# Kernel tuning notes

Hardware: AMD Instinct MI355X
Metric: run time of the kernel (lower is better)

## Reference

```python
import jax, jax.numpy as jnp
import numpy as np

D_MODEL = 256

def setup_inputs() -> dict:
    key = jax.random.key(0)
    k_x, k_wqkv, k_bqkv, k_wp, k_bp = jax.random.split(key, 5)
    B, T, d = 4, 4096, D_MODEL
    bound_qkv = 1.0 / np.sqrt(d)
    return {
        "x": jax.random.normal(k_x, (B, T, d), dtype=jnp.float32),
        "W_qkv": jax.random.uniform(k_wqkv, (d, 3 * d), jnp.float32, -bound_qkv, bound_qkv),
        "b_qkv": jax.random.uniform(k_bqkv, (3 * d,), jnp.float32, -bound_qkv, bound_qkv),
        "W_proj": jax.random.uniform(k_wp, (d, d), jnp.float32, -bound_qkv, bound_qkv),
        "b_proj": jax.random.uniform(k_bp, (d,), jnp.float32, -bound_qkv, bound_qkv),
    }

def reference(x, W_qkv, b_qkv, W_proj, b_proj):
    B, T, d = x.shape
    qkv = x @ W_qkv + b_qkv                       # (B, T, 3d)
    q, k, v = jnp.split(qkv, 3, axis=-1)          # each (B, T, d)
    scale = 1.0 / np.sqrt(d).astype(np.float32)
    scores = jnp.einsum('btd,bsd->bts', q, k) * scale   # (B, T, T)
    causal = jnp.tril(jnp.ones((T, T), dtype=bool))     # allowed positions
    scores = jnp.where(causal, scores, -jnp.inf)
    weights = jax.nn.softmax(scores, axis=-1)           # (B, T, T)
    ctx = jnp.einsum('bts,bsd->btd', weights, v)        # (B, T, d)
    return ctx @ W_proj + b_proj
```

## Files before the change

### kernel.cpp

```cpp
#include <hip/hip_runtime.h>
#include <math.h>

#define TT 4096
#define BB 4
#define DM 256
#define NSEG_B 80

typedef __attribute__((ext_vector_type(8))) short short8;
typedef __attribute__((ext_vector_type(4))) short short4v;
typedef __attribute__((ext_vector_type(4))) float f32x4;

#define MFMA16(a, b, c) __builtin_amdgcn_mfma_f32_16x16x32_bf16(a, b, c, 0, 0, 0)

#define GL2LDS(gp, lp) __builtin_amdgcn_global_load_lds( \
    (const __attribute__((address_space(1))) unsigned int*)(gp), \
    (__attribute__((address_space(3))) unsigned int*)(lp), 16, 0, 0)

__device__ __forceinline__ short f2b(float f) {
    union { float f; unsigned u; } v; v.f = f;
    unsigned r = v.u + 0x7FFFu + ((v.u >> 16) & 1u);
    return (short)(r >> 16);
}

__global__ __launch_bounds__(256) void transpose_cast2(
    const float* __restrict__ W1, short* __restrict__ Wt1,
    const float* __restrict__ W2, short* __restrict__ Wt2)
{
    __shared__ float T[64 * 68];
    const int tid = threadIdx.x;
    const int by = blockIdx.y;
    const float* W; short* Wt; int N, n0;
    if (by < 12) { W = W1; Wt = Wt1; N = 768; n0 = by * 64; }
    else         { W = W2; Wt = Wt2; N = 256; n0 = (by - 12) * 64; }
    const int k0 = blockIdx.x * 64;
#pragma unroll
    for (int it = 0; it < 4; ++it) {
        int idx = tid + it * 256;
        int r = idx >> 4, c4 = idx & 15;
        *(float4*)&T[r * 68 + c4 * 4] =
            *(const float4*)&W[(size_t)(k0 + r) * N + n0 + c4 * 4];
    }
    __syncthreads();
#pragma unroll
    for (int it = 0; it < 4; ++it) {
        int idx = tid + it * 256;
        int n = idx >> 4, c4 = idx & 15;
        short4v t;
#pragma unroll
        for (int j = 0; j < 4; ++j) t[j] = f2b(T[(c4 * 4 + j) * 68 + n]);
        *(short4v*)&Wt[(size_t)(n0 + n) * 256 + k0 + c4 * 4] = t;
    }
}

__global__ __launch_bounds__(256) void qkv_gemm(
    const float* __restrict__ x, const short* __restrict__ Bt,
    const float* __restrict__ bias, short* __restrict__ qkvb,
    short* __restrict__ VtG)
{
    __shared__ short As[16384];
    __shared__ short Bs[16384];
    __shared__ short Ts[64 * 72];

    const int tid = threadIdx.x;
    const int w = tid >> 6, lane = tid & 63;
    const int l15 = lane & 15, quad = lane >> 4;
    const int m0 = blockIdx.x * 64;
    const int nsup = blockIdx.y * 384;

#pragma unroll
    for (int it = 0; it < 8; ++it) {
        int idx = tid + it * 256;
        int row = ((idx >> 9) << 4) + (idx & 15);
        int col = ((idx >> 6) & 7) * 32 + ((idx >> 4) & 3) * 8;
        const float* src = &x[(size_t)(m0 + row) * 256 + col];
        float4 u = *(const float4*)src, u2 = *(const float4*)(src + 4);
        short8 t;
        t[0] = f2b(u.x);  t[1] = f2b(u.y);  t[2] = f2b(u.z);  t[3] = f2b(u.w);
        t[4] = f2b(u2.x); t[5] = f2b(u2.y); t[6] = f2b(u2.z); t[7] = f2b(u2.w);
        *(short8*)&As[idx * 8] = t;
    }

    for (int t6 = 0; t6 < 6; ++t6) {
        const int n0 = nsup + t6 * 64;
#pragma unroll
        for (int it = 0; it < 8; ++it) {
            int idx = tid + it * 256;
            int n = ((idx >> 9) << 4) + (idx & 15);
            int col = ((idx >> 6) & 7) * 32 + ((idx >> 4) & 3) * 8;
            *(short8*)&Bs[idx * 8] = *(const short8*)&Bt[(size_t)(n0 + n) * 256 + col];
        }
        __syncthreads();

        f32x4 acc[4];
#pragma unroll
        for (int t = 0; t < 4; ++t) acc[t] = (f32x4){0.f, 0.f, 0.f, 0.f};
#pragma unroll
        for (int k0 = 0; k0 < 8; ++k0) {
            short8 a = *(const short8*)&As[((w * 8 + k0) * 64 + lane) * 8];
#pragma unroll
            for (int nt = 0; nt < 4; ++nt) {
                short8 bb = *(const short8*)&Bs[((nt * 8 + k0) * 64 + lane) * 8];
                acc[nt] = MFMA16(a, bb, acc[nt]);
            }
        }

        if (n0 < 512) {
#pragma unroll
            for (int nt = 0; nt < 4; ++nt) {
                int n = n0 + nt * 16 + l15;
                float bv = bias[n];
#pragma unroll
                for (int r = 0; r < 4; ++r)
                    qkvb[(size_t)(m0 + w * 16 + quad * 4 + r) * 768 + n]
                        = f2b(acc[nt][r] + bv);
            }
            __syncthreads();
        } else {
#pragma unroll
            for (int nt = 0; nt < 4; ++nt) {
                int n = n0 + nt * 16 + l15;
                float bv = bias[n];
#pragma unroll
                for (int r = 0; r < 4; ++r)
                    Ts[(nt * 16 + l15) * 72 + w * 16 + quad * 4 + r]
                        = f2b(acc[nt][r] + bv);
            }
            __syncthreads();
            const int d  = tid >> 2;
            const int c  = tid & 3;
            short8 v0 = *(const short8*)&Ts[d * 72 + c * 16];
            short8 v1 = *(const short8*)&Ts[d * 72 + c * 16 + 8];
            const int bg = m0 >> 12, key0 = (m0 & 4095) + c * 16;
            short* dst = &VtG[((size_t)bg * 256 + (n0 - 512) + d) * 4096 + key0];
            *(short8*)dst = v0;
            *(short8*)(dst + 8) = v1;
        }
    }
}

__global__ __launch_bounds__(256, 2) void flash_mfma(
    const short* __restrict__ qkv,
    const short* __restrict__ VtG,
    float* __restrict__ Opart,
    float* __restrict__ L)
{
    __shared__ short Ks[2][8192];
    __shared__ short Vs[2][8192];
    __shared__ short Ps[4096];

    const int tid = threadIdx.x;
    const int w = tid >> 6, lane = tid & 63;
    const int l15 = lane & 15, quad = lane >> 4;

    const int b = blockIdx.x & 3;
    const int e = (NSEG_B - 1) - (blockIdx.x >> 2);
    const int lid = b * NSEG_B + e;
    int gg = 0;
    while (gg < 3 && e >= 4 * (gg + 1) * (gg + 2)) ++gg;
    int off = e - 4 * gg * (gg + 1);
    int qt = 8 * gg + off / (gg + 1);
    int s  = off - (off / (gg + 1)) * (gg + 1);
    const int kb_lo = s * 32;
    const int kb_hi = min(kb_lo + 32, 4 * (qt + 1));
    const int nunits = kb_hi - kb_lo;

    const size_t base = (size_t)b * TT * 768;
    const int row0 = qt * 128;

    short8 aq[2][8];
#pragma unroll
    for (int rs = 0; rs < 2; ++rs) {
        const short* qrow = &qkv[base + (size_t)(row0 + rs * 64 + w * 16 + l15) * 768 + quad * 8];
#pragma unroll
        for (int k0 = 0; k0 < 8; ++k0)
            aq[rs][k0] = *(const short8*)&qrow[k0 * 32];
    }

#pragma unroll
    for (int it = 0; it < 4; ++it) {
        int idx = tid + it * 256;
        int row = ((idx >> 9) << 4) + (idx & 15);
        int col = ((idx >> 6) & 7) * 32 + ((idx >> 4) & 3) * 8;
        GL2LDS(&qkv[base + (size_t)(kb_lo * 32 + row) * 768 + 256 + col], &Ks[0][idx * 8]);
        int d  = ((idx >> 6) << 4) + (idx & 15);
        int kc = ((idx >> 4) & 3) * 8;
        GL2LDS(&VtG[((size_t)b * 256 + d) * 4096 + kb_lo * 32 + kc], &Vs[0][idx * 8]);
    }

    f32x4 o[2][16];
#pragma unroll
    for (int rs = 0; rs < 2; ++rs)
#pragma unroll
        for (int c = 0; c < 16; ++c) o[rs][c] = (f32x4){0.f, 0.f, 0.f, 0.f};
    float l_acc[2][4] = {{0.f, 0.f, 0.f, 0.f}, {0.f, 0.f, 0.f, 0.f}};

    for (int u = 0; u < nunits; ++u) {
        const int p = u & 1;
        const int j0 = (kb_lo + u) * 32;

        __syncthreads();

        if (u + 1 < nunits) {
            const int j0n = j0 + 32;
#pragma unroll
            for (int it = 0; it < 4; ++it) {
                int idx = tid + it * 256;
                int row = ((idx >> 9) << 4) + (idx & 15);
                int col = ((idx >> 6) & 7) * 32 + ((idx >> 4) & 3) * 8;
                GL2LDS(&qkv[base + (size_t)(j0n + row) * 768 + 256 + col], &Ks[p ^ 1][idx * 8]);
                int d  = ((idx >> 6) << 4) + (idx & 15);
                int kc = ((idx >> 4) & 3) * 8;
                GL2LDS(&VtG[((size_t)b * 256 + d) * 4096 + j0n + kc], &Vs[p ^ 1][idx * 8]);
            }
        }

        f32x4 s4[2][2];
#pragma unroll
        for (int rs = 0; rs < 2; ++rs)
#pragma unroll
            for (int nt = 0; nt < 2; ++nt) s4[rs][nt] = (f32x4){0.f, 0.f, 0.f, 0.f};
#pragma unroll
        for (int k0 = 0; k0 < 8; ++k0) {
#pragma unroll
            for (int nt = 0; nt < 2; ++nt) {
                short8 bb = *(const short8*)&Ks[p][((nt * 8 + k0) * 64 + lane) * 8];
                s4[0][nt] = MFMA16(aq[0][k0], bb, s4[0][nt]);
                s4[1][nt] = MFMA16(aq[1][k0], bb, s4[1][nt]);
            }
        }

#pragma unroll
        for (int rs = 0; rs < 2; ++rs) {
#pragma unroll
            for (int r = 0; r < 4; ++r) {
                const int rg = row0 + rs * 64 + w * 16 + quad * 4 + r;
#pragma unroll
                for (int nt = 0; nt < 2; ++nt) {
                    int jg = j0 + nt * 16 + l15;
                    float xx = s4[rs][nt][r] * 0.0625f;
                    if (jg > rg) xx = -INFINITY;
                    float pv = __expf(fminf(xx, 30.f));
                    l_acc[rs][r] += pv;
                    Ps[((rs * 4 + w) * 64 + (nt * 2 + (l15 >> 3)) * 16 + quad * 4 + r) * 8
                       + (l15 & 7)] = f2b(pv);
                }
            }
        }

        {
            short8 a0 = *(const short8*)&Ps[((0 * 4 + w) * 64 + lane) * 8];
            short8 a1 = *(const short8*)&Ps[((1 * 4 + w) * 64 + lane) * 8];
#pragma unroll
            for (int ct = 0; ct < 16; ++ct) {
                short8 bb = *(const short8*)&Vs[p][(ct * 64 + lane) * 8];
                o[0][ct] = MFMA16(a0, bb, o[0][ct]);
                o[1][ct] = MFMA16(a1, bb, o[1][ct]);
            }
        }
    }

#pragma unroll
    for (int rs = 0; rs < 2; ++rs)
#pragma unroll
        for (int r = 0; r < 4; ++r) {
            float l = l_acc[rs][r];
            l += __shfl_xor(l, 1); l += __shfl_xor(l, 2);
            l += __shfl_xor(l, 4); l += __shfl_xor(l, 8);
            if (l15 == 0)
                L[(size_t)lid * 128 + rs * 64 + w * 16 + quad * 4 + r] = l;
        }
    const size_t ob = (size_t)lid * (128 * 256);
#pragma unroll
    for (int rs = 0; rs < 2; ++rs)
#pragma unroll
        for (int r = 0; r < 4; ++r) {
            int lr = rs * 64 + w * 16 + quad * 4 + r;
#pragma unroll
            for (int c = 0; c < 16; ++c)
                Opart[ob + (size_t)lr * 256 + c * 16 + l15] = o[rs][c][r];
        }
}

__global__ __launch_bounds__(256) void proj_gemm(
    const float* __restrict__ Opart, const float* __restrict__ L,
    const short* __restrict__ Bt, const float* __restrict__ bias,
    float* __restrict__ out)
{
    __shared__ short As[16384];
    __shared__ short Bs[16384];
    __shared__ float Linv[64];

    const int tid = threadIdx.x;
    const int w = tid >> 6, lane = tid & 63;
    const int l15 = lane & 15, quad = lane >> 4;
    const int t = blockIdx.x;
    const int b = t >> 6, q64 = t & 63;
    const int qt = q64 >> 1, half = q64 & 1;
    const int gg = qt >> 3, rr = qt & 7;
    const int sbase = b * NSEG_B + 4 * gg * (gg + 1) + rr * (gg + 1);
    const int nseg = gg + 1;
    const int m0 = t * 64;
    const int ro = half * 64;

    if (tid < 64) {
        float l = 0.f;
#pragma unroll
        for (int s2 = 0; s2 < 4; ++s2)
            if (s2 < nseg) l += L[(size_t)(sbase + s2) * 128 + ro + tid];
        Linv[tid] = 1.f / l;
    }
    __syncthreads();

#pragma unroll
    for (int it = 0; it < 8; ++it) {
        int idx = tid + it * 256;
        int row = ((idx >> 9) << 4) + (idx & 15);
        int col = ((idx >> 6) & 7) * 32 + ((idx >> 4) & 3) * 8;
        float a8[8] = {0.f, 0.f, 0.f, 0.f, 0.f, 0.f, 0.f, 0.f};
#pragma unroll
        for (int s2 = 0; s2 < 4; ++s2) {
            if (s2 < nseg) {
                const float* src = &Opart[(size_t)(sbase + s2) * 32768
                                          + (size_t)(ro + row) * 256 + col];
                float4 u = *(const float4*)src, u2 = *(const float4*)(src + 4);
                a8[0] += u.x;  a8[1] += u.y;  a8[2] += u.z;  a8[3] += u.w;
                a8[4] += u2.x; a8[5] += u2.y; a8[6] += u2.z; a8[7] += u2.w;
            }
        }
        float inv = Linv[row];
        short8 t8;
#pragma unroll
        for (int j = 0; j < 8; ++j) t8[j] = f2b(a8[j] * inv);
        *(short8*)&As[idx * 8] = t8;
    }

    for (int t2 = 0; t2 < 2; ++t2) {
        const int n0 = blockIdx.y * 128 + t2 * 64;
#pragma unroll
        for (int it = 0; it < 8; ++it) {
            int idx = tid + it * 256;
            int n = ((idx >> 9) << 4) + (idx & 15);
            int col = ((idx >> 6) & 7) * 32 + ((idx >> 4) & 3) * 8;
            *(short8*)&Bs[idx * 8] = *(const short8*)&Bt[(size_t)(n0 + n) * 256 + col];
        }
        __syncthreads();

        f32x4 acc[4];
#pragma unroll
        for (int tt = 0; tt < 4; ++tt) acc[tt] = (f32x4){0.f, 0.f, 0.f, 0.f};
#pragma unroll
        for (int k0 = 0; k0 < 8; ++k0) {
            short8 a = *(const short8*)&As[((w * 8 + k0) * 64 + lane) * 8];
#pragma unroll
            for (int nt = 0; nt < 4; ++nt) {
                short8 bb = *(const short8*)&Bs[((nt * 8 + k0) * 64 + lane) * 8];
                acc[nt] = MFMA16(a, bb, acc[nt]);
            }
        }
#pragma unroll
        for (int nt = 0; nt < 4; ++nt) {
            int n = n0 + nt * 16 + l15;
            float bv = bias[n];
#pragma unroll
            for (int r = 0; r < 4; ++r)
                out[(size_t)(m0 + w * 16 + quad * 4 + r) * 256 + n] = acc[nt][r] + bv;
        }
        __syncthreads();
    }
}

extern "C" void kernel_launch(void* const* d_in, const int* in_sizes, int n_in,
                              void* d_out, int out_size, void* d_ws, size_t ws_size,
                              hipStream_t stream)
{
    const float* x     = (const float*)d_in[0];
    const float* Wqkv  = (const float*)d_in[1];
    const float* bqkv  = (const float*)d_in[2];
    const float* Wproj = (const float*)d_in[3];
    const float* bproj = (const float*)d_in[4];
    float* out = (float*)d_out;

    const size_t M = (size_t)BB * TT;
    short* qkv_b = (short*)d_ws;
    short* Wt1   = qkv_b + M * 768;
    short* Wt2   = Wt1 + (size_t)768 * 256;
    short* VtG   = Wt2 + (size_t)256 * 256;
    float* Opart = (float*)(VtG + (size_t)BB * 256 * 4096);
    float* L     = Opart + (size_t)320 * 128 * 256;

    dim3 blk(256);
    transpose_cast2<<<dim3(4, 16), blk, 0, stream>>>(Wqkv, Wt1, Wproj, Wt2);
    qkv_gemm<<<dim3(256, 2), blk, 0, stream>>>(x, Wt1, bqkv, qkv_b, VtG);
    flash_mfma<<<dim3(BB * NSEG_B), blk, 0, stream>>>(qkv_b, VtG, Opart, L);
    proj_gemm<<<dim3(256, 2), blk, 0, stream>>>(Opart, L, Wt2, bproj, out);
}
```

Before: 220.0 us.

## Split causal attention into finer key segments and store partial outputs in bf16

Changes the split-K decomposition of the flash attention kernel from up to 32 key blocks per segment (80 segments per batch) to up to 16 (144 segments per batch). This raises the block count to 576 for better load balance and CU occupancy on the causal triangle. The partial output buffer becomes bf16 instead of fp32, which halves the write and read traffic added by having more segments. In exchange the projection kernel has more partials to sum, up to 8, and the partials lose precision before normalization.

After: 227.6 us. 1.03x slower.

```diff
diff --git a/kernel.cpp b/kernel.cpp
--- a/kernel.cpp
+++ b/kernel.cpp
@@ -4,7 +4,7 @@
 #define TT 4096
 #define BB 4
 #define DM 256
-#define NSEG_B 80
+#define NSEG_B 144
 
 typedef __attribute__((ext_vector_type(8))) short short8;
 typedef __attribute__((ext_vector_type(4))) short short4v;
@@ -20,6 +20,11 @@
     union { float f; unsigned u; } v; v.f = f;
     unsigned r = v.u + 0x7FFFu + ((v.u >> 16) & 1u);
     return (short)(r >> 16);
+}
+__device__ __forceinline__ float b2f(short h) {
+    union { unsigned u; float f; } v;
+    v.u = ((unsigned)(unsigned short)h) << 16;
+    return v.f;
 }
 
 __global__ __launch_bounds__(256) void transpose_cast2(
@@ -141,7 +146,7 @@
 __global__ __launch_bounds__(256, 2) void flash_mfma(
     const short* __restrict__ qkv,
     const short* __restrict__ VtG,
-    float* __restrict__ Opart,
+    short* __restrict__ Opart,
     float* __restrict__ L)
 {
     __shared__ short Ks[2][8192];
@@ -155,13 +160,13 @@
     const int b = blockIdx.x & 3;
     const int e = (NSEG_B - 1) - (blockIdx.x >> 2);
     const int lid = b * NSEG_B + e;
-    int gg = 0;
-    while (gg < 3 && e >= 4 * (gg + 1) * (gg + 2)) ++gg;
-    int off = e - 4 * gg * (gg + 1);
-    int qt = 8 * gg + off / (gg + 1);
-    int s  = off - (off / (gg + 1)) * (gg + 1);
-    const int kb_lo = s * 32;
-    const int kb_hi = min(kb_lo + 32, 4 * (qt + 1));
+    int p5 = 0;
+    while (p5 < 7 && e >= 2 * (p5 + 1) * (p5 + 2)) ++p5;
+    int off = e - 2 * p5 * (p5 + 1);
+    int qt = 4 * p5 + off / (p5 + 1);
+    int s  = off - (off / (p5 + 1)) * (p5 + 1);
+    const int kb_lo = s * 16;
+    const int kb_hi = min(kb_lo + 16, 4 * (qt + 1));
     const int nunits = kb_hi - kb_lo;
 
     const size_t base = (size_t)b * TT * 768;
@@ -277,12 +282,12 @@
             int lr = rs * 64 + w * 16 + quad * 4 + r;
 #pragma unroll
             for (int c = 0; c < 16; ++c)
-                Opart[ob + (size_t)lr * 256 + c * 16 + l15] = o[rs][c][r];
+                Opart[ob + (size_t)lr * 256 + c * 16 + l15] = f2b(o[rs][c][r]);
         }
 }
 
 __global__ __launch_bounds__(256) void proj_gemm(
-    const float* __restrict__ Opart, const float* __restrict__ L,
+    const short* __restrict__ Opart, const float* __restrict__ L,
     const short* __restrict__ Bt, const float* __restrict__ bias,
     float* __restrict__ out)
 {
@@ -296,16 +301,16 @@
     const int t = blockIdx.x;
     const int b = t >> 6, q64 = t & 63;
     const int qt = q64 >> 1, half = q64 & 1;
-    const int gg = qt >> 3, rr = qt & 7;
-    const int sbase = b * NSEG_B + 4 * gg * (gg + 1) + rr * (gg + 1);
-    const int nseg = gg + 1;
+    const int p5 = qt >> 2;
+    const int sbase = b * NSEG_B + 2 * p5 * (p5 + 1) + (qt & 3) * (p5 + 1);
+    const int nseg = p5 + 1;
     const int m0 = t * 64;
     const int ro = half * 64;
 
     if (tid < 64) {
         float l = 0.f;
 #pragma unroll
-        for (int s2 = 0; s2 < 4; ++s2)
+        for (int s2 = 0; s2 < 8; ++s2)
             if (s2 < nseg) l += L[(size_t)(sbase + s2) * 128 + ro + tid];
         Linv[tid] = 1.f / l;
     }
@@ -318,13 +323,12 @@
         int col = ((idx >> 6) & 7) * 32 + ((idx >> 4) & 3) * 8;
         float a8[8] = {0.f, 0.f, 0.f, 0.f, 0.f, 0.f, 0.f, 0.f};
 #pragma unroll
-        for (int s2 = 0; s2 < 4; ++s2) {
+        for (int s2 = 0; s2 < 8; ++s2) {
             if (s2 < nseg) {
-                const float* src = &Opart[(size_t)(sbase + s2) * 32768
-                                          + (size_t)(ro + row) * 256 + col];
-                float4 u = *(const float4*)src, u2 = *(const float4*)(src + 4);
-                a8[0] += u.x;  a8[1] += u.y;  a8[2] += u.z;  a8[3] += u.w;
-                a8[4] += u2.x; a8[5] += u2.y; a8[6] += u2.z; a8[7] += u2.w;
+                short8 v = *(const short8*)&Opart[(size_t)(sbase + s2) * 32768
+                                                  + (size_t)(ro + row) * 256 + col];
+#pragma unroll
+                for (int j = 0; j < 8; ++j) a8[j] += b2f(v[j]);
             }
         }
         float inv = Linv[row];
@@ -381,16 +385,16 @@
     float* out = (float*)d_out;
 
     const size_t M = (size_t)BB * TT;
-    short* qkv_b = (short*)d_ws;
-    short* Wt1   = qkv_b + M * 768;
-    short* Wt2   = Wt1 + (size_t)768 * 256;
-    short* VtG   = Wt2 + (size_t)256 * 256;
-    float* Opart = (float*)(VtG + (size_t)BB * 256 * 4096);
-    float* L     = Opart + (size_t)320 * 128 * 256;
+    short* qkv_b  = (short*)d_ws;
+    short* Wt1    = qkv_b + M * 768;
+    short* Wt2    = Wt1 + (size_t)768 * 256;
+    short* VtG    = Wt2 + (size_t)256 * 256;
+    short* OpartB = VtG + (size_t)BB * 256 * 4096;
+    float* L      = (float*)(OpartB + (size_t)4 * NSEG_B * 128 * 256);
 
     dim3 blk(256);
     transpose_cast2<<<dim3(4, 16), blk, 0, stream>>>(Wqkv, Wt1, Wproj, Wt2);
     qkv_gemm<<<dim3(256, 2), blk, 0, stream>>>(x, Wt1, bqkv, qkv_b, VtG);
-    flash_mfma<<<dim3(BB * NSEG_B), blk, 0, stream>>>(qkv_b, VtG, Opart, L);
-    proj_gemm<<<dim3(256, 2), blk, 0, stream>>>(Opart, L, Wt2, bproj, out);
-}
+    flash_mfma<<<dim3(BB * NSEG_B), blk, 0, stream>>>(qkv_b, VtG, OpartB, L);
+    proj_gemm<<<dim3(256, 2), blk, 0, stream>>>(OpartB, L, Wt2, bproj, out);
+}
```
